# Optimization experiments

Measured on AMD Instinct MI355X. Metric: run time of the kernel, lower is better.

## Reference

```python
import jax, jax.numpy as jnp
import numpy as np

NE = 14          # NUM_ELEMENTS
NC = 20          # world channels
CLONER = 13      # cloner element one-hot channel
CA = NE + 3      # cloner_assigns channel (=17)
B, H, W = 32, 256, 256

# torch.roll equivalents (dims 2 = H, dims 3 = W)
def _below(x):  return jnp.roll(x, -1, axis=2)
def _above(x):  return jnp.roll(x,  1, axis=2)
def _left(x):   return jnp.roll(x,  1, axis=3)
def _right(x):  return jnp.roll(x, -1, axis=3)
DIRS = (_below, _above, _left, _right)


def setup_inputs() -> dict:
    key = jax.random.key(0)
    k1, k2, k3, k4, k5 = jax.random.split(key, 5)
    # one-hot element channels [B, NE, H, W]
    ids = jax.random.randint(k1, (B, H, W), 0, NE)
    onehot = jnp.transpose(jax.nn.one_hot(ids, NE, dtype=jnp.float32), (0, 3, 1, 2))
    # extra scalar channels [B, NC-NE, H, W]
    extra = jax.random.normal(k2, (B, NC - NE, H, W), dtype=jnp.float32)
    world = jnp.concatenate([onehot, extra], axis=1)
    # cloner_assigns channel holds element ids stored as floats
    ca_init = jax.random.randint(k3, (B, 1, H, W), 0, NE).astype(jnp.float32)
    world = world.at[:, CA:CA + 1].set(ca_init)
    elem_vecs = jax.random.normal(k4, (NE, NC), dtype=jnp.float32)  # embedding table
    info = jax.random.normal(k5, (B,), dtype=jnp.float32)
    return {"world": world, "elem_vecs": elem_vecs, "info": info}


def _forward(world, elem_vecs):
    # labels = argmax over element one-hot channels, kept as [B,1,H,W]
    labels = jnp.argmax(world[:, :NE], axis=1)[:, None].astype(world.dtype)
    is_not_cloner = ~(world[:, CLONER:CLONER + 1] > 0.5)
    # Pass 1: sequentially propagate a label into empty cloner assignment slots.
    for d in DIRS:
        ca = world[:, CA:CA + 1]
        is_cloner_empty = (~is_not_cloner) & ((ca == 0.0) | (ca == 13.0))
        # torch: ~(is_cloner_empty|is_not_cloner)*ca + is_cloner_empty*dir_labels
        new_ca = jnp.where(is_cloner_empty, d(labels),
                           jnp.where(is_not_cloner, jnp.zeros((), world.dtype), ca))
        world = world.at[:, CA:CA + 1].set(new_ca)
    # Embedding lookup of assigned element vectors: [B,H,W,NC] -> [B,NC,H,W]
    vec = jnp.transpose(elem_vecs[world[:, CA].astype(jnp.int32)], (0, 3, 1, 2))
    # Pass 2: sequentially write cloner's element vector into adjacent empty cells.
    for d in DIRS:
        ca = world[:, CA:CA + 1]
        is_cloner = world[:, CLONER:CLONER + 1] > 0.5
        is_empty = world[:, 0:1] > 0.5
        mask = d(is_cloner & (ca != 0.0) & (ca != 13.0)) & is_empty  # [B,1,H,W]
        world = jnp.where(mask, d(vec), world)
    return world


def reference(world, elem_vecs, info):
    return (_forward(world, elem_vecs), info)
```

## Files before the change

kernel.cpp:

```cpp
#include <hip/hip_runtime.h>

namespace {
constexpr int kNE = 14;
constexpr int kNC = 20;
constexpr int kCloner = 13;
constexpr int kCA = 17;
constexpr int kB = 32;
constexpr int kH = 256;
constexpr int kW = 256;

constexpr int kT = 32;
constexpr int kE = kT + 4;
constexpr int kLW = 40;
constexpr int kThreads = 256;
constexpr size_t kPlane = (size_t)kH * kW;
}


__global__ __launch_bounds__(kThreads)
void k_pack(const float* __restrict__ world, const float* __restrict__ info,
            float* __restrict__ out, unsigned short* __restrict__ pack)
{
    const int g = blockIdx.x * kThreads + threadIdx.x;
    const int b = g >> 14;
    const int rem = g & 16383;
    const size_t off = (size_t)rem << 2;
    const float* wb = world + (size_t)b * kNC * kPlane;

    int lab[4] = {0, 0, 0, 0};
    #pragma unroll
    for (int c = 0; c < kNE; ++c) {
        const float4 v = *reinterpret_cast<const float4*>(wb + (size_t)c * kPlane + off);
        if (v.x > 0.5f) lab[0] = c;
        if (v.y > 0.5f) lab[1] = c;
        if (v.z > 0.5f) lab[2] = c;
        if (v.w > 0.5f) lab[3] = c;
    }
    const float4 ca4 = *reinterpret_cast<const float4*>(wb + (size_t)kCA * kPlane + off);
    const int cai[4] = {(int)ca4.x, (int)ca4.y, (int)ca4.z, (int)ca4.w};
    unsigned short p[4];
    #pragma unroll
    for (int j = 0; j < 4; ++j) {
        unsigned short q = (unsigned short)(lab[j] | (cai[j] << 8));
        if (lab[j] == kCloner) q |= 16;
        if (lab[j] == 0)       q |= 32;
        p[j] = q;
    }
    ushort4 st; st.x = p[0]; st.y = p[1]; st.z = p[2]; st.w = p[3];
    *reinterpret_cast<ushort4*>(pack + (size_t)b * kPlane + off) = st;

    if (g < kB) out[(size_t)kB * kNC * kPlane + g] = info[g];
}

__device__ __forceinline__ unsigned bc_step(unsigned s, unsigned ns,
                                            const unsigned short* __restrict__ vb) {
    if ((ns & 2u) && (s & 1u)) {
        const unsigned v = (ns >> 4) & 15u;
        return (s & 0x00F0u) | vb[v] | (v << 8) | 0x1000u;
    }
    return s;
}

__global__ __launch_bounds__(kThreads)
void k_apply(const float* __restrict__ world, const float* __restrict__ ev,
             const unsigned short* __restrict__ pack, float* __restrict__ out)
{
    __shared__ unsigned short sPack[kE][kLW];
    __shared__ unsigned short sA[kE][kLW];
    __shared__ float sEV[kNE * kNC];
    __shared__ unsigned short sVbits[kNE];

    const int tid = threadIdx.x;
    const int b  = blockIdx.z;
    const int h0 = blockIdx.y * kT;
    const int w0 = blockIdx.x * kT;
    const float* wb = world + (size_t)b * kNC * kPlane;
    float*       ob = out   + (size_t)b * kNC * kPlane;
    const unsigned short* pb = pack + (size_t)b * kPlane;

    const int th  = tid >> 3;
    const int tw4 = (tid & 7) * 4;
    const size_t off4 = (size_t)(h0 + th) * kW + (w0 + tw4);
    float4 extra[5];
    extra[0] = *reinterpret_cast<const float4*>(wb + (size_t)14 * kPlane + off4);
    extra[1] = *reinterpret_cast<const float4*>(wb + (size_t)15 * kPlane + off4);
    extra[2] = *reinterpret_cast<const float4*>(wb + (size_t)16 * kPlane + off4);
    extra[3] = *reinterpret_cast<const float4*>(wb + (size_t)18 * kPlane + off4);
    extra[4] = *reinterpret_cast<const float4*>(wb + (size_t)19 * kPlane + off4);

    for (int i = tid; i < kNE * kNC; i += kThreads) sEV[i] = ev[i];
    if (tid < kNE) {
        const float e0  = ev[tid * kNC + 0];
        const float c13 = ev[tid * kNC + kCloner];
        const float c17 = ev[tid * kNC + kCA];
        unsigned short vb = 0;
        if (e0 > 0.5f) vb |= 1;
        if (c13 > 0.5f && c17 != 0.0f && c17 != 13.0f) vb |= 2;
        sVbits[tid] = vb;
    }

    for (int idx = tid; idx < kE * 10; idx += kThreads) {
        const int eh = idx / 10;
        const int k  = idx - eh * 10;
        const int h = (h0 + eh - 2) & (kH - 1);
        const int w = (w0 - 4 + 4 * k) & (kW - 1);
        const ushort4 v = *reinterpret_cast<const ushort4*>(pb + (size_t)h * kW + w);
        sPack[eh][4 * k + 0] = v.x;
        sPack[eh][4 * k + 1] = v.y;
        sPack[eh][4 * k + 2] = v.z;
        sPack[eh][4 * k + 3] = v.w;
    }
    __syncthreads();

    for (int idx = tid; idx < 34 * 34; idx += kThreads) {
        const int eh = idx / 34 + 1;
        const int lw = idx % 34 + 3;
        const unsigned short p = sPack[eh][lw];
        int fca = 0;
        if (p & 16) {
            int ca = (p >> 8) & 15;
            if (ca == 0 || ca == 13) ca = sPack[eh + 1][lw] & 15;
            if (ca == 0 || ca == 13) ca = sPack[eh - 1][lw] & 15;
            if (ca == 0 || ca == 13) ca = sPack[eh][lw - 1] & 15;
            if (ca == 0 || ca == 13) ca = sPack[eh][lw + 1] & 15;
            fca = ca;
        }
        unsigned short s = (unsigned short)(fca << 4);
        if (p & 32) s |= 1;
        if ((p & 16) && fca != 0 && fca != 13) s |= 2;
        sA[eh][lw] = s;
    }
    __syncthreads();

    {
        const int eh  = th + 2;
        const int lw0 = tw4 + 4;

        unsigned s0[3][6];
        #pragma unroll
        for (int r = 0; r < 3; ++r)
            #pragma unroll
            for (int c = 0; c < 6; ++c)
                s0[r][c] = sA[eh - 1 + r][lw0 - 1 + c];

        unsigned s1[2][6];
        #pragma unroll
        for (int r = 0; r < 2; ++r)
            #pragma unroll
            for (int c = 0; c < 6; ++c)
                s1[r][c] = bc_step(s0[r][c], s0[r + 1][c], sVbits);

        unsigned s2[6];
        #pragma unroll
        for (int c = 0; c < 6; ++c)
            s2[c] = bc_step(s1[1][c], s1[0][c], sVbits);

        unsigned s3[5];
        #pragma unroll
        for (int c = 0; c < 5; ++c)
            s3[c] = bc_step(s2[c + 1], s2[c], sVbits);

        unsigned s4[4];
        #pragma unroll
        for (int j = 0; j < 4; ++j)
            s4[j] = bc_step(s3[j], s3[j + 1], sVbits);

        bool  o[4]; int src[4]; float fcaf[4]; int lb[4];
        #pragma unroll
        for (int j = 0; j < 4; ++j) {
            o[j]    = (s4[j] & 0x1000u) != 0;
            src[j]  = (s4[j] >> 8) & 15;
            fcaf[j] = (float)((s4[j] >> 4) & 15);
            lb[j]   = sPack[eh][lw0 + j] & 15;
        }

        #pragma unroll
        for (int c = 0; c < kNC; ++c) {
            float base[4];
            if (c < kNE) {
                #pragma unroll
                for (int j = 0; j < 4; ++j) base[j] = (lb[j] == c) ? 1.0f : 0.0f;
            } else if (c == kCA) {
                #pragma unroll
                for (int j = 0; j < 4; ++j) base[j] = fcaf[j];
            } else {
                const float4 v = extra[c < kCA ? c - kNE : c - kNE - 1];
                base[0] = v.x; base[1] = v.y; base[2] = v.z; base[3] = v.w;
            }
            float4 r;
            r.x = o[0] ? sEV[src[0] * kNC + c] : base[0];
            r.y = o[1] ? sEV[src[1] * kNC + c] : base[1];
            r.z = o[2] ? sEV[src[2] * kNC + c] : base[2];
            r.w = o[3] ? sEV[src[3] * kNC + c] : base[3];
            *reinterpret_cast<float4*>(ob + (size_t)c * kPlane + off4) = r;
        }
    }
}

__global__ __launch_bounds__(kThreads)
void bc_fused(const float* __restrict__ world, const float* __restrict__ ev,
              const float* __restrict__ info, float* __restrict__ out)
{
    __shared__ unsigned short sPack[kE][kLW];
    __shared__ unsigned short sA[kE][kLW];
    __shared__ unsigned short sB[kE][kLW];
    __shared__ float sEV[kNE * kNC];
    __shared__ unsigned short sVbits[kNE];

    const int tid = threadIdx.x;
    const int b  = blockIdx.z;
    const int h0 = blockIdx.y * kT;
    const int w0 = blockIdx.x * kT;
    const float* wb = world + (size_t)b * kNC * kPlane;
    float*       ob = out   + (size_t)b * kNC * kPlane;

    for (int i = tid; i < kNE * kNC; i += kThreads) sEV[i] = ev[i];
    if (tid < kNE) {
        const float e0  = ev[tid * kNC + 0];
        const float c13 = ev[tid * kNC + kCloner];
        const float c17 = ev[tid * kNC + kCA];
        unsigned short vb = 0;
        if (e0 > 0.5f) vb |= 1;
        if (c13 > 0.5f && c17 != 0.0f && c17 != 13.0f) vb |= 2;
        sVbits[tid] = vb;
    }
    for (int idx = tid; idx < kE * 10; idx += kThreads) {
        const int eh = idx / 10;
        const int k  = idx - eh * 10;
        const int h = (h0 + eh - 2) & (kH - 1);
        const int w = (w0 - 4 + 4 * k) & (kW - 1);
        const size_t off = (size_t)h * kW + w;
        int lab[4] = {0,0,0,0};
        #pragma unroll
        for (int c = 0; c < kNE; ++c) {
            const float4 v = *reinterpret_cast<const float4*>(wb + (size_t)c * kPlane + off);
            if (v.x > 0.5f) lab[0] = c;
            if (v.y > 0.5f) lab[1] = c;
            if (v.z > 0.5f) lab[2] = c;
            if (v.w > 0.5f) lab[3] = c;
        }
        const float4 ca4 = *reinterpret_cast<const float4*>(wb + (size_t)kCA * kPlane + off);
        const int cai[4] = {(int)ca4.x, (int)ca4.y, (int)ca4.z, (int)ca4.w};
        #pragma unroll
        for (int j = 0; j < 4; ++j) {
            unsigned short p = (unsigned short)(lab[j] | (cai[j] << 8));
            if (lab[j] == kCloner) p |= 16;
            if (lab[j] == 0)       p |= 32;
            sPack[eh][4 * k + j] = p;
        }
    }
    __syncthreads();
    for (int idx = tid; idx < 34 * 34; idx += kThreads) {
        const int eh = idx / 34 + 1;
        const int lw = idx % 34 + 3;
        const unsigned short p = sPack[eh][lw];
        int fca = 0;
        if (p & 16) {
            int ca = (p >> 8) & 15;
            if (ca == 0 || ca == 13) ca = sPack[eh + 1][lw] & 15;
            if (ca == 0 || ca == 13) ca = sPack[eh - 1][lw] & 15;
            if (ca == 0 || ca == 13) ca = sPack[eh][lw - 1] & 15;
            if (ca == 0 || ca == 13) ca = sPack[eh][lw + 1] & 15;
            fca = ca;
        }
        unsigned short s = (unsigned short)(fca << 4);
        if (p & 32) s |= 1;
        if ((p & 16) && fca != 0 && fca != 13) s |= 2;
        sA[eh][lw] = s;
    }
    unsigned short (*prev)[kLW] = sA;
    unsigned short (*next)[kLW] = sB;
    {
        const int dh[4]   = {1, -1, 0, 0};
        const int dw[4]   = {0, 0, -1, 1};
        const int rhlo[4] = {1, 2, 2, 2};
        const int rhhi[4] = {33, 33, 33, 33};
        const int rwlo[4] = {3, 3, 4, 4};
        const int rwhi[4] = {36, 36, 36, 35};
        for (int d = 0; d < 4; ++d) {
            __syncthreads();
            const int nh = rhhi[d] - rhlo[d] + 1;
            const int nw = rwhi[d] - rwlo[d] + 1;
            for (int idx = tid; idx < nh * nw; idx += kThreads) {
                const int eh = rhlo[d] + idx / nw;
                const int lw = rwlo[d] + idx % nw;
                unsigned short s = prev[eh][lw];
                const unsigned short ns = prev[eh + dh[d]][lw + dw[d]];
                if ((ns & 2) && (s & 1)) {
                    const int v = (ns >> 4) & 15;
                    s = (unsigned short)((s & 0x00F0) | sVbits[v] | (v << 8) | 0x1000);
                }
                next[eh][lw] = s;
            }
            unsigned short (*t)[kLW] = prev; prev = next; next = t;
        }
    }
    __syncthreads();
    {
        const int th = tid >> 3;
        const int tw = (tid & 7) * 4;
        const int eh = th + 2;
        const size_t off = (size_t)(h0 + th) * kW + (w0 + tw);
        bool  o[4]; int src[4]; float fcaf[4]; int lb[4];
        #pragma unroll
        for (int j = 0; j < 4; ++j) {
            const unsigned short s = prev[eh][tw + 4 + j];
            o[j]    = (s & 0x1000) != 0;
            src[j]  = (s >> 8) & 15;
            fcaf[j] = (float)((s >> 4) & 15);
            lb[j]   = sPack[eh][tw + 4 + j] & 15;
        }
        #pragma unroll
        for (int c = 0; c < kNC; ++c) {
            float base[4];
            if (c >= kNE && c != kCA) {
                const float4 v = *reinterpret_cast<const float4*>(wb + (size_t)c * kPlane + off);
                base[0] = v.x; base[1] = v.y; base[2] = v.z; base[3] = v.w;
            } else if (c == kCA) {
                base[0] = fcaf[0]; base[1] = fcaf[1]; base[2] = fcaf[2]; base[3] = fcaf[3];
            } else {
                #pragma unroll
                for (int j = 0; j < 4; ++j) base[j] = (lb[j] == c) ? 1.0f : 0.0f;
            }
            float4 r;
            r.x = o[0] ? sEV[src[0] * kNC + c] : base[0];
            r.y = o[1] ? sEV[src[1] * kNC + c] : base[1];
            r.z = o[2] ? sEV[src[2] * kNC + c] : base[2];
            r.w = o[3] ? sEV[src[3] * kNC + c] : base[3];
            *reinterpret_cast<float4*>(ob + (size_t)c * kPlane + off) = r;
        }
    }
    if (blockIdx.x == 0 && blockIdx.y == 0 && blockIdx.z == 0 && tid < kB) {
        out[(size_t)kB * kNC * kPlane + tid] = info[tid];
    }
}

extern "C" void kernel_launch(void* const* d_in, const int* in_sizes, int n_in,
                              void* d_out, int out_size, void* d_ws, size_t ws_size,
                              hipStream_t stream) {
    const float* world = (const float*)d_in[0];
    const float* ev    = (const float*)d_in[1];
    const float* info  = (const float*)d_in[2];
    float* out = (float*)d_out;
    const size_t packBytes = (size_t)kB * kPlane * sizeof(unsigned short);
    if (ws_size >= packBytes) {
        unsigned short* pack = (unsigned short*)d_ws;
        k_pack<<<dim3((kB * (int)kPlane / 4) / kThreads), kThreads, 0, stream>>>(world, info, out, pack);
        k_apply<<<dim3(kW / kT, kH / kT, kB), kThreads, 0, stream>>>(world, ev, pack, out);
    } else {
        bc_fused<<<dim3(kW / kT, kH / kT, kB), kThreads, 0, stream>>>(world, ev, info, out);
    }
}
```

Measured before the change: 72.14 us.

## Copy unchanged channels in pack kernel and scatter only overridden pixels

The pack kernel now streams all unchanged world channels straight into the output while computing labels, and stores a one-byte packed label/assignment map instead of two bytes. The second kernel writes only the cloner-assign channel densely and scatters element vectors only to pixels that pass-2 overrides. This aims to make the heavy traffic a simple coalesced copy and to shrink the second kernel's work. It relies on stream ordering for the overwrite and adds uncoalesced scalar stores for overridden pixels.

```diff
diff --git a/kernel.cpp b/kernel.cpp
--- a/kernel.cpp
+++ b/kernel.cpp
@@ -18,14 +18,15 @@
 
 
 __global__ __launch_bounds__(kThreads)
-void k_pack(const float* __restrict__ world, const float* __restrict__ info,
-            float* __restrict__ out, unsigned short* __restrict__ pack)
+void k_pack_copy(const float* __restrict__ world, const float* __restrict__ info,
+                 float* __restrict__ out, unsigned char* __restrict__ pack)
 {
     const int g = blockIdx.x * kThreads + threadIdx.x;
     const int b = g >> 14;
     const int rem = g & 16383;
     const size_t off = (size_t)rem << 2;
     const float* wb = world + (size_t)b * kNC * kPlane;
+    float*       ob = out   + (size_t)b * kNC * kPlane;
 
     int lab[4] = {0, 0, 0, 0};
     #pragma unroll
@@ -35,19 +36,21 @@
         if (v.y > 0.5f) lab[1] = c;
         if (v.z > 0.5f) lab[2] = c;
         if (v.w > 0.5f) lab[3] = c;
+        *reinterpret_cast<float4*>(ob + (size_t)c * kPlane + off) = v;
+    }
+    #pragma unroll
+    for (int c = kNE; c < kNC; ++c) {
+        if (c == kCA) continue;
+        const float4 v = *reinterpret_cast<const float4*>(wb + (size_t)c * kPlane + off);
+        *reinterpret_cast<float4*>(ob + (size_t)c * kPlane + off) = v;
     }
     const float4 ca4 = *reinterpret_cast<const float4*>(wb + (size_t)kCA * kPlane + off);
-    const int cai[4] = {(int)ca4.x, (int)ca4.y, (int)ca4.z, (int)ca4.w};
-    unsigned short p[4];
-    #pragma unroll
-    for (int j = 0; j < 4; ++j) {
-        unsigned short q = (unsigned short)(lab[j] | (cai[j] << 8));
-        if (lab[j] == kCloner) q |= 16;
-        if (lab[j] == 0)       q |= 32;
-        p[j] = q;
-    }
-    ushort4 st; st.x = p[0]; st.y = p[1]; st.z = p[2]; st.w = p[3];
-    *reinterpret_cast<ushort4*>(pack + (size_t)b * kPlane + off) = st;
+    uchar4 p;
+    p.x = (unsigned char)(lab[0] | ((int)ca4.x << 4));
+    p.y = (unsigned char)(lab[1] | ((int)ca4.y << 4));
+    p.z = (unsigned char)(lab[2] | ((int)ca4.z << 4));
+    p.w = (unsigned char)(lab[3] | ((int)ca4.w << 4));
+    *reinterpret_cast<uchar4*>(pack + (size_t)b * kPlane + off) = p;
 
     if (g < kB) out[(size_t)kB * kNC * kPlane + g] = info[g];
 }
@@ -62,10 +65,10 @@
 }
 
 __global__ __launch_bounds__(kThreads)
-void k_apply(const float* __restrict__ world, const float* __restrict__ ev,
-             const unsigned short* __restrict__ pack, float* __restrict__ out)
+void k_ca(const float* __restrict__ ev, const unsigned char* __restrict__ pack,
+          float* __restrict__ out)
 {
-    __shared__ unsigned short sPack[kE][kLW];
+    __shared__ unsigned char  sP[kE][kLW];
     __shared__ unsigned short sA[kE][kLW];
     __shared__ float sEV[kNE * kNC];
     __shared__ unsigned short sVbits[kNE];
@@ -74,19 +77,8 @@
     const int b  = blockIdx.z;
     const int h0 = blockIdx.y * kT;
     const int w0 = blockIdx.x * kT;
-    const float* wb = world + (size_t)b * kNC * kPlane;
-    float*       ob = out   + (size_t)b * kNC * kPlane;
-    const unsigned short* pb = pack + (size_t)b * kPlane;
-
-    const int th  = tid >> 3;
-    const int tw4 = (tid & 7) * 4;
-    const size_t off4 = (size_t)(h0 + th) * kW + (w0 + tw4);
-    float4 extra[5];
-    extra[0] = *reinterpret_cast<const float4*>(wb + (size_t)14 * kPlane + off4);
-    extra[1] = *reinterpret_cast<const float4*>(wb + (size_t)15 * kPlane + off4);
-    extra[2] = *reinterpret_cast<const float4*>(wb + (size_t)16 * kPlane + off4);
-    extra[3] = *reinterpret_cast<const float4*>(wb + (size_t)18 * kPlane + off4);
-    extra[4] = *reinterpret_cast<const float4*>(wb + (size_t)19 * kPlane + off4);
+    float* ob = out + (size_t)b * kNC * kPlane;
+    const unsigned char* pb = pack + (size_t)b * kPlane;
 
     for (int i = tid; i < kNE * kNC; i += kThreads) sEV[i] = ev[i];
     if (tid < kNE) {
@@ -104,95 +96,89 @@
         const int k  = idx - eh * 10;
         const int h = (h0 + eh - 2) & (kH - 1);
         const int w = (w0 - 4 + 4 * k) & (kW - 1);
-        const ushort4 v = *reinterpret_cast<const ushort4*>(pb + (size_t)h * kW + w);
-        sPack[eh][4 * k + 0] = v.x;
-        sPack[eh][4 * k + 1] = v.y;
-        sPack[eh][4 * k + 2] = v.z;
-        sPack[eh][4 * k + 3] = v.w;
+        const uchar4 v = *reinterpret_cast<const uchar4*>(pb + (size_t)h * kW + w);
+        sP[eh][4 * k + 0] = v.x;
+        sP[eh][4 * k + 1] = v.y;
+        sP[eh][4 * k + 2] = v.z;
+        sP[eh][4 * k + 3] = v.w;
     }
     __syncthreads();
 
     for (int idx = tid; idx < 34 * 34; idx += kThreads) {
         const int eh = idx / 34 + 1;
         const int lw = idx % 34 + 3;
-        const unsigned short p = sPack[eh][lw];
+        const unsigned p = sP[eh][lw];
+        const unsigned lb = p & 15u;
         int fca = 0;
-        if (p & 16) {
-            int ca = (p >> 8) & 15;
-            if (ca == 0 || ca == 13) ca = sPack[eh + 1][lw] & 15;
-            if (ca == 0 || ca == 13) ca = sPack[eh - 1][lw] & 15;
-            if (ca == 0 || ca == 13) ca = sPack[eh][lw - 1] & 15;
-            if (ca == 0 || ca == 13) ca = sPack[eh][lw + 1] & 15;
+        if (lb == kCloner) {
+            int ca = (int)(p >> 4);
+            if (ca == 0 || ca == 13) ca = sP[eh + 1][lw] & 15;
+            if (ca == 0 || ca == 13) ca = sP[eh - 1][lw] & 15;
+            if (ca == 0 || ca == 13) ca = sP[eh][lw - 1] & 15;
+            if (ca == 0 || ca == 13) ca = sP[eh][lw + 1] & 15;
             fca = ca;
         }
         unsigned short s = (unsigned short)(fca << 4);
-        if (p & 32) s |= 1;
-        if ((p & 16) && fca != 0 && fca != 13) s |= 2;
+        if (lb == 0) s |= 1;
+        if (lb == kCloner && fca != 0 && fca != 13) s |= 2;
         sA[eh][lw] = s;
     }
     __syncthreads();
 
+    const int th  = tid >> 3;
+    const int tw4 = (tid & 7) * 4;
+    const int eh  = th + 2;
+    const int lw0 = tw4 + 4;
+    const size_t off4 = (size_t)(h0 + th) * kW + (w0 + tw4);
+
+    unsigned s0[3][6];
+    #pragma unroll
+    for (int r = 0; r < 3; ++r)
+        #pragma unroll
+        for (int c = 0; c < 6; ++c)
+            s0[r][c] = sA[eh - 1 + r][lw0 - 1 + c];
+
+    unsigned s1[2][6];
+    #pragma unroll
+    for (int r = 0; r < 2; ++r)
+        #pragma unroll
+        for (int c = 0; c < 6; ++c)
+            s1[r][c] = bc_step(s0[r][c], s0[r + 1][c], sVbits);
+
+    unsigned s2[6];
+    #pragma unroll
+    for (int c = 0; c < 6; ++c)
+        s2[c] = bc_step(s1[1][c], s1[0][c], sVbits);
+
+    unsigned s3[5];
+    #pragma unroll
+    for (int c = 0; c < 5; ++c)
+        s3[c] = bc_step(s2[c + 1], s2[c], sVbits);
+
+    unsigned s4[4];
+    #pragma unroll
+    for (int j = 0; j < 4; ++j)
+        s4[j] = bc_step(s3[j], s3[j + 1], sVbits);
+
     {
-        const int eh  = th + 2;
-        const int lw0 = tw4 + 4;
-
-        unsigned s0[3][6];
-        #pragma unroll
-        for (int r = 0; r < 3; ++r)
+        float4 r17;
+        r17.x = (s4[0] & 0x1000u) ? sEV[((s4[0] >> 8) & 15) * kNC + kCA] : (float)((s4[0] >> 4) & 15);
+        r17.y = (s4[1] & 0x1000u) ? sEV[((s4[1] >> 8) & 15) * kNC + kCA] : (float)((s4[1] >> 4) & 15);
+        r17.z = (s4[2] & 0x1000u) ? sEV[((s4[2] >> 8) & 15) * kNC + kCA] : (float)((s4[2] >> 4) & 15);
+        r17.w = (s4[3] & 0x1000u) ? sEV[((s4[3] >> 8) & 15) * kNC + kCA] : (float)((s4[3] >> 4) & 15);
+        *reinterpret_cast<float4*>(ob + (size_t)kCA * kPlane + off4) = r17;
+    }
+
+    #pragma unroll
+    for (int j = 0; j < 4; ++j) {
+        if (s4[j] & 0x1000u) {
+            const float* vv = &sEV[((s4[j] >> 8) & 15) * kNC];
+            float* op = ob + off4 + j;
             #pragma unroll
-            for (int c = 0; c < 6; ++c)
-                s0[r][c] = sA[eh - 1 + r][lw0 - 1 + c];
-
-        unsigned s1[2][6];
-        #pragma unroll
-        for (int r = 0; r < 2; ++r)
-            #pragma unroll
-            for (int c = 0; c < 6; ++c)
-                s1[r][c] = bc_step(s0[r][c], s0[r + 1][c], sVbits);
-
-        unsigned s2[6];
-        #pragma unroll
-        for (int c = 0; c < 6; ++c)
-            s2[c] = bc_step(s1[1][c], s1[0][c], sVbits);
-
-        unsigned s3[5];
-        #pragma unroll
-        for (int c = 0; c < 5; ++c)
-            s3[c] = bc_step(s2[c + 1], s2[c], sVbits);
-
-        unsigned s4[4];
-        #pragma unroll
-        for (int j = 0; j < 4; ++j)
-            s4[j] = bc_step(s3[j], s3[j + 1], sVbits);
-
-        bool  o[4]; int src[4]; float fcaf[4]; int lb[4];
-        #pragma unroll
-        for (int j = 0; j < 4; ++j) {
-            o[j]    = (s4[j] & 0x1000u) != 0;
-            src[j]  = (s4[j] >> 8) & 15;
-            fcaf[j] = (float)((s4[j] >> 4) & 15);
-            lb[j]   = sPack[eh][lw0 + j] & 15;
-        }
-
-        #pragma unroll
-        for (int c = 0; c < kNC; ++c) {
-            float base[4];
-            if (c < kNE) {
-                #pragma unroll
-                for (int j = 0; j < 4; ++j) base[j] = (lb[j] == c) ? 1.0f : 0.0f;
-            } else if (c == kCA) {
-                #pragma unroll
-                for (int j = 0; j < 4; ++j) base[j] = fcaf[j];
-            } else {
-                const float4 v = extra[c < kCA ? c - kNE : c - kNE - 1];
-                base[0] = v.x; base[1] = v.y; base[2] = v.z; base[3] = v.w;
+            for (int c = 0; c < kNC; ++c) {
+                if (c == kCA) continue;
+                op[(size_t)c * kPlane] = vv[c];
             }
-            float4 r;
-            r.x = o[0] ? sEV[src[0] * kNC + c] : base[0];
-            r.y = o[1] ? sEV[src[1] * kNC + c] : base[1];
-            r.z = o[2] ? sEV[src[2] * kNC + c] : base[2];
-            r.w = o[3] ? sEV[src[3] * kNC + c] : base[3];
-            *reinterpret_cast<float4*>(ob + (size_t)c * kPlane + off4) = r;
         }
     }
 }
@@ -342,11 +328,11 @@
     const float* ev    = (const float*)d_in[1];
     const float* info  = (const float*)d_in[2];
     float* out = (float*)d_out;
-    const size_t packBytes = (size_t)kB * kPlane * sizeof(unsigned short);
+    const size_t packBytes = (size_t)kB * kPlane;
     if (ws_size >= packBytes) {
-        unsigned short* pack = (unsigned short*)d_ws;
-        k_pack<<<dim3((kB * (int)kPlane / 4) / kThreads), kThreads, 0, stream>>>(world, info, out, pack);
-        k_apply<<<dim3(kW / kT, kH / kT, kB), kThreads, 0, stream>>>(world, ev, pack, out);
+        unsigned char* pack = (unsigned char*)d_ws;
+        k_pack_copy<<<dim3((kB * (int)kPlane / 4) / kThreads), kThreads, 0, stream>>>(world, info, out, pack);
+        k_ca<<<dim3(kW / kT, kH / kT, kB), kThreads, 0, stream>>>(ev, pack, out);
     } else {
         bc_fused<<<dim3(kW / kT, kH / kT, kB), kThreads, 0, stream>>>(world, ev, info, out);
     }
```

After: 86.71 us. 1.2x slower.

## Pack labels into bytes and tile k_apply by full-width row strips

Applied to the files above, without the earlier changes.

The intermediate pack buffer shrinks from 16-bit to 8-bit entries, with the label in the low nibble and the cloner assignment in the high nibble. The cloner and empty flags are now recomputed from the label. k_apply switches from 32x32 tiles with a 2-cell halo on all sides to strips of 4 full-width rows with a 2-row halo. Horizontal wraparound is handled inside shared memory, so redundant halo loads and pack-buffer traffic go down. The trade-off is that the row-halo overhead per strip is now proportionally larger (8 rows loaded to produce 4).

```diff
diff --git a/kernel.cpp b/kernel.cpp
--- a/kernel.cpp
+++ b/kernel.cpp
@@ -9,17 +9,19 @@
 constexpr int kH = 256;
 constexpr int kW = 256;
 
+constexpr int kSH = 4;
+constexpr int kThreads = 256;
+constexpr size_t kPlane = (size_t)kH * kW;
+
 constexpr int kT = 32;
 constexpr int kE = kT + 4;
 constexpr int kLW = 40;
-constexpr int kThreads = 256;
-constexpr size_t kPlane = (size_t)kH * kW;
 }
 
 
 __global__ __launch_bounds__(kThreads)
 void k_pack(const float* __restrict__ world, const float* __restrict__ info,
-            float* __restrict__ out, unsigned short* __restrict__ pack)
+            float* __restrict__ out, unsigned char* __restrict__ pack)
 {
     const int g = blockIdx.x * kThreads + threadIdx.x;
     const int b = g >> 14;
@@ -37,17 +39,12 @@
         if (v.w > 0.5f) lab[3] = c;
     }
     const float4 ca4 = *reinterpret_cast<const float4*>(wb + (size_t)kCA * kPlane + off);
-    const int cai[4] = {(int)ca4.x, (int)ca4.y, (int)ca4.z, (int)ca4.w};
-    unsigned short p[4];
-    #pragma unroll
-    for (int j = 0; j < 4; ++j) {
-        unsigned short q = (unsigned short)(lab[j] | (cai[j] << 8));
-        if (lab[j] == kCloner) q |= 16;
-        if (lab[j] == 0)       q |= 32;
-        p[j] = q;
-    }
-    ushort4 st; st.x = p[0]; st.y = p[1]; st.z = p[2]; st.w = p[3];
-    *reinterpret_cast<ushort4*>(pack + (size_t)b * kPlane + off) = st;
+    uchar4 p;
+    p.x = (unsigned char)(lab[0] | ((int)ca4.x << 4));
+    p.y = (unsigned char)(lab[1] | ((int)ca4.y << 4));
+    p.z = (unsigned char)(lab[2] | ((int)ca4.z << 4));
+    p.w = (unsigned char)(lab[3] | ((int)ca4.w << 4));
+    *reinterpret_cast<uchar4*>(pack + (size_t)b * kPlane + off) = p;
 
     if (g < kB) out[(size_t)kB * kNC * kPlane + g] = info[g];
 }
@@ -63,24 +60,24 @@
 
 __global__ __launch_bounds__(kThreads)
 void k_apply(const float* __restrict__ world, const float* __restrict__ ev,
-             const unsigned short* __restrict__ pack, float* __restrict__ out)
+             const unsigned char* __restrict__ pack, float* __restrict__ out)
 {
-    __shared__ unsigned short sPack[kE][kLW];
-    __shared__ unsigned short sA[kE][kLW];
+    __shared__ unsigned char  sP[kSH + 4][kW];
+    __shared__ unsigned short sA[kSH + 2][kW];
     __shared__ float sEV[kNE * kNC];
     __shared__ unsigned short sVbits[kNE];
 
     const int tid = threadIdx.x;
-    const int b  = blockIdx.z;
-    const int h0 = blockIdx.y * kT;
-    const int w0 = blockIdx.x * kT;
+    const int y0 = blockIdx.x * kSH;
+    const int b  = blockIdx.y;
     const float* wb = world + (size_t)b * kNC * kPlane;
     float*       ob = out   + (size_t)b * kNC * kPlane;
-    const unsigned short* pb = pack + (size_t)b * kPlane;
-
-    const int th  = tid >> 3;
-    const int tw4 = (tid & 7) * 4;
-    const size_t off4 = (size_t)(h0 + th) * kW + (w0 + tw4);
+    const unsigned char* pb = pack + (size_t)b * kPlane;
+
+    const int th   = tid >> 6;
+    const int col4 = (tid & 63) * 4;
+    const size_t off4 = (size_t)(y0 + th) * kW + col4;
+
     float4 extra[5];
     extra[0] = *reinterpret_cast<const float4*>(wb + (size_t)14 * kPlane + off4);
     extra[1] = *reinterpret_cast<const float4*>(wb + (size_t)15 * kPlane + off4);
@@ -99,101 +96,95 @@
         sVbits[tid] = vb;
     }
 
-    for (int idx = tid; idx < kE * 10; idx += kThreads) {
-        const int eh = idx / 10;
-        const int k  = idx - eh * 10;
-        const int h = (h0 + eh - 2) & (kH - 1);
-        const int w = (w0 - 4 + 4 * k) & (kW - 1);
-        const ushort4 v = *reinterpret_cast<const ushort4*>(pb + (size_t)h * kW + w);
-        sPack[eh][4 * k + 0] = v.x;
-        sPack[eh][4 * k + 1] = v.y;
-        sPack[eh][4 * k + 2] = v.z;
-        sPack[eh][4 * k + 3] = v.w;
+    for (int idx = tid; idx < (kSH + 4) * (kW / 4); idx += kThreads) {
+        const int r  = idx >> 6;
+        const int c4 = (idx & 63) * 4;
+        const int h  = (y0 - 2 + r) & (kH - 1);
+        *reinterpret_cast<uchar4*>(&sP[r][c4]) =
+            *reinterpret_cast<const uchar4*>(pb + (size_t)h * kW + c4);
     }
     __syncthreads();
 
-    for (int idx = tid; idx < 34 * 34; idx += kThreads) {
-        const int eh = idx / 34 + 1;
-        const int lw = idx % 34 + 3;
-        const unsigned short p = sPack[eh][lw];
+    for (int idx = tid; idx < (kSH + 2) * kW; idx += kThreads) {
+        const int r   = idx >> 8;
+        const int col = idx & 255;
+        const int pr  = r + 1;
+        const unsigned p  = sP[pr][col];
+        const unsigned lb = p & 15u;
         int fca = 0;
-        if (p & 16) {
-            int ca = (p >> 8) & 15;
-            if (ca == 0 || ca == 13) ca = sPack[eh + 1][lw] & 15;
-            if (ca == 0 || ca == 13) ca = sPack[eh - 1][lw] & 15;
-            if (ca == 0 || ca == 13) ca = sPack[eh][lw - 1] & 15;
-            if (ca == 0 || ca == 13) ca = sPack[eh][lw + 1] & 15;
+        if (lb == kCloner) {
+            int ca = (int)(p >> 4);
+            if (ca == 0 || ca == 13) ca = sP[pr + 1][col] & 15;
+            if (ca == 0 || ca == 13) ca = sP[pr - 1][col] & 15;
+            if (ca == 0 || ca == 13) ca = sP[pr][(col - 1) & 255] & 15;
+            if (ca == 0 || ca == 13) ca = sP[pr][(col + 1) & 255] & 15;
             fca = ca;
         }
         unsigned short s = (unsigned short)(fca << 4);
-        if (p & 32) s |= 1;
-        if ((p & 16) && fca != 0 && fca != 13) s |= 2;
-        sA[eh][lw] = s;
+        if (lb == 0) s |= 1;
+        if (lb == kCloner && fca != 0 && fca != 13) s |= 2;
+        sA[r][col] = s;
     }
     __syncthreads();
 
-    {
-        const int eh  = th + 2;
-        const int lw0 = tw4 + 4;
-
-        unsigned s0[3][6];
-        #pragma unroll
-        for (int r = 0; r < 3; ++r)
+    const int ar = th + 1;
+    unsigned s0[3][6];
+    #pragma unroll
+    for (int r = 0; r < 3; ++r)
+        #pragma unroll
+        for (int c = 0; c < 6; ++c)
+            s0[r][c] = sA[ar - 1 + r][(col4 - 1 + c) & 255];
+
+    unsigned s1[2][6];
+    #pragma unroll
+    for (int r = 0; r < 2; ++r)
+        #pragma unroll
+        for (int c = 0; c < 6; ++c)
+            s1[r][c] = bc_step(s0[r][c], s0[r + 1][c], sVbits);
+
+    unsigned s2[6];
+    #pragma unroll
+    for (int c = 0; c < 6; ++c)
+        s2[c] = bc_step(s1[1][c], s1[0][c], sVbits);
+
+    unsigned s3[5];
+    #pragma unroll
+    for (int c = 0; c < 5; ++c)
+        s3[c] = bc_step(s2[c + 1], s2[c], sVbits);
+
+    unsigned s4[4];
+    #pragma unroll
+    for (int j = 0; j < 4; ++j)
+        s4[j] = bc_step(s3[j], s3[j + 1], sVbits);
+
+    bool  o[4]; int src[4]; float fcaf[4]; int lb[4];
+    #pragma unroll
+    for (int j = 0; j < 4; ++j) {
+        o[j]    = (s4[j] & 0x1000u) != 0;
+        src[j]  = (s4[j] >> 8) & 15;
+        fcaf[j] = (float)((s4[j] >> 4) & 15);
+        lb[j]   = sP[th + 2][col4 + j] & 15;
+    }
+
+    #pragma unroll
+    for (int c = 0; c < kNC; ++c) {
+        float base[4];
+        if (c < kNE) {
             #pragma unroll
-            for (int c = 0; c < 6; ++c)
-                s0[r][c] = sA[eh - 1 + r][lw0 - 1 + c];
-
-        unsigned s1[2][6];
-        #pragma unroll
-        for (int r = 0; r < 2; ++r)
+            for (int j = 0; j < 4; ++j) base[j] = (lb[j] == c) ? 1.0f : 0.0f;
+        } else if (c == kCA) {
             #pragma unroll
-            for (int c = 0; c < 6; ++c)
-                s1[r][c] = bc_step(s0[r][c], s0[r + 1][c], sVbits);
-
-        unsigned s2[6];
-        #pragma unroll
-        for (int c = 0; c < 6; ++c)
-            s2[c] = bc_step(s1[1][c], s1[0][c], sVbits);
-
-        unsigned s3[5];
-        #pragma unroll
-        for (int c = 0; c < 5; ++c)
-            s3[c] = bc_step(s2[c + 1], s2[c], sVbits);
-
-        unsigned s4[4];
-        #pragma unroll
-        for (int j = 0; j < 4; ++j)
-            s4[j] = bc_step(s3[j], s3[j + 1], sVbits);
-
-        bool  o[4]; int src[4]; float fcaf[4]; int lb[4];
-        #pragma unroll
-        for (int j = 0; j < 4; ++j) {
-            o[j]    = (s4[j] & 0x1000u) != 0;
-            src[j]  = (s4[j] >> 8) & 15;
-            fcaf[j] = (float)((s4[j] >> 4) & 15);
-            lb[j]   = sPack[eh][lw0 + j] & 15;
-        }
-
-        #pragma unroll
-        for (int c = 0; c < kNC; ++c) {
-            float base[4];
-            if (c < kNE) {
-                #pragma unroll
-                for (int j = 0; j < 4; ++j) base[j] = (lb[j] == c) ? 1.0f : 0.0f;
-            } else if (c == kCA) {
-                #pragma unroll
-                for (int j = 0; j < 4; ++j) base[j] = fcaf[j];
-            } else {
-                const float4 v = extra[c < kCA ? c - kNE : c - kNE - 1];
-                base[0] = v.x; base[1] = v.y; base[2] = v.z; base[3] = v.w;
-            }
-            float4 r;
-            r.x = o[0] ? sEV[src[0] * kNC + c] : base[0];
-            r.y = o[1] ? sEV[src[1] * kNC + c] : base[1];
-            r.z = o[2] ? sEV[src[2] * kNC + c] : base[2];
-            r.w = o[3] ? sEV[src[3] * kNC + c] : base[3];
-            *reinterpret_cast<float4*>(ob + (size_t)c * kPlane + off4) = r;
-        }
+            for (int j = 0; j < 4; ++j) base[j] = fcaf[j];
+        } else {
+            const float4 v = extra[c < kCA ? c - kNE : c - kNE - 1];
+            base[0] = v.x; base[1] = v.y; base[2] = v.z; base[3] = v.w;
+        }
+        float4 r;
+        r.x = o[0] ? sEV[src[0] * kNC + c] : base[0];
+        r.y = o[1] ? sEV[src[1] * kNC + c] : base[1];
+        r.z = o[2] ? sEV[src[2] * kNC + c] : base[2];
+        r.w = o[3] ? sEV[src[3] * kNC + c] : base[3];
+        *reinterpret_cast<float4*>(ob + (size_t)c * kPlane + off4) = r;
     }
 }
 
@@ -342,11 +333,11 @@
     const float* ev    = (const float*)d_in[1];
     const float* info  = (const float*)d_in[2];
     float* out = (float*)d_out;
-    const size_t packBytes = (size_t)kB * kPlane * sizeof(unsigned short);
+    const size_t packBytes = (size_t)kB * kPlane;
     if (ws_size >= packBytes) {
-        unsigned short* pack = (unsigned short*)d_ws;
+        unsigned char* pack = (unsigned char*)d_ws;
         k_pack<<<dim3((kB * (int)kPlane / 4) / kThreads), kThreads, 0, stream>>>(world, info, out, pack);
-        k_apply<<<dim3(kW / kT, kH / kT, kB), kThreads, 0, stream>>>(world, ev, pack, out);
+        k_apply<<<dim3(kH / kSH, kB), kThreads, 0, stream>>>(world, ev, pack, out);
     } else {
         bc_fused<<<dim3(kW / kT, kH / kT, kB), kThreads, 0, stream>>>(world, ev, info, out);
     }
```

Result: faster. 69.31 us (-3.9%).
